# Optimization experiments

Measured on AMD Instinct MI355X. Metric: run time of the kernel, lower is better.

The kernel has to match this reference:

```python
import jax, jax.numpy as jnp
import numpy as np

# ---- module geometry ----
BULK = 64          # bulk (J2) integration points, 3 comps each
COH = 32           # cohesive integration points, 2 comps each
LS = BULK * 3 + COH * 2  # = 256, material layer width

# ---- J2 plasticity material constants (plane-stress, linear isotropic hardening) ----
E_MOD = 200.0
NU = 0.3
SY0 = 2.0
HARD = 10.0
G_MOD = E_MOD / (2.0 * (1.0 + NU))
_c = E_MOD / (1.0 - NU * NU)
C_EL = np.array([[_c, _c * NU, 0.0], [_c * NU, _c, 0.0], [0.0, 0.0, _c * (1.0 - NU) / 2.0]], dtype=np.float32)
C_INV = np.linalg.inv(C_EL).astype(np.float32)

# ---- Turon cohesive-zone constants (bilinear damage law) ----
K_PEN = 50.0       # penalty stiffness
DELTA0 = 0.1       # damage-onset effective jump
DELTAF = 1.0       # full-failure effective jump


def j2_update(eps, epsp, epbar):
    # eps, epsp: [B,P,3]; epbar: [B,P]. Radial-return with linear hardening.
    sig_tr = jnp.einsum('bpi,ji->bpj', eps - epsp, jnp.asarray(C_EL))
    s1, s2, s12 = sig_tr[..., 0], sig_tr[..., 1], sig_tr[..., 2]
    seq = jnp.sqrt(jnp.maximum(s1 * s1 - s1 * s2 + s2 * s2 + 3.0 * s12 * s12, 1e-12))
    f = seq - (SY0 + HARD * epbar)
    plastic = f > 0.0
    dep = jnp.where(plastic, f / (3.0 * G_MOD + HARD), 0.0)
    r = (SY0 + HARD * (epbar + dep)) / seq
    sig = jnp.where(plastic[..., None], r[..., None] * sig_tr, sig_tr)
    epsp_new = jnp.where(plastic[..., None], eps - jnp.einsum('bpj,ij->bpi', sig, jnp.asarray(C_INV)), epsp)
    return sig, epsp_new, epbar + dep


def coh_update(jump, hist):
    # jump: [B,P,2] (normal, shear); hist: [B,P] max effective jump (damage history).
    dn, ds = jump[..., 0], jump[..., 1]
    lam = jnp.sqrt(jnp.maximum(jnp.maximum(dn, 0.0) ** 2 + ds * ds, 1e-12))
    hist_new = jnp.maximum(hist, lam)
    dmg = jnp.clip(DELTAF * (hist_new - DELTA0) / (jnp.maximum(hist_new, 1e-12) * (DELTAF - DELTA0)), 0.0, 1.0)
    tn = K_PEN * dn * jnp.where(dn > 0.0, 1.0 - dmg, 1.0)  # compression is undamaged
    ts = (1.0 - dmg) * K_PEN * ds
    return jnp.stack([tn, ts], axis=-1), hist_new


def setup_inputs() -> dict:
    key = jax.random.key(0)
    k1, k2, k3 = jax.random.split(key, 3)
    x = jax.random.normal(k1, (256, 1024, 16), dtype=jnp.float32)
    W1 = jax.random.normal(k2, (LS, 16), dtype=jnp.float32) * 0.1
    W2 = jax.random.normal(k3, (16, LS), dtype=jnp.float32) * 0.1
    return {"x": x, "W1": W1, "W2": W2}


def reference(x, W1, W2):
    B, T, F = x.shape
    # fc1 applied to every (batch, time) slice (original loops; here one GEMM)
    h = jnp.einsum('btf,lf->btl', x, W1)  # [B,T,LS]
    h_t = jnp.transpose(h, (1, 0, 2))     # [T,B,LS] for the time scan

    epsp0 = jnp.zeros((B, BULK, 3), dtype=x.dtype)
    epbar0 = jnp.zeros((B, BULK), dtype=x.dtype)
    hist0 = jnp.zeros((B, COH), dtype=x.dtype)

    def step(carry, ht):
        epsp, epbar, hist = carry
        eps = ht[:, : BULK * 3].reshape(B, BULK, 3)
        jmp = ht[:, BULK * 3:].reshape(B, COH, 2)
        sig, epsp, epbar = j2_update(eps, epsp, epbar)   # update + commit per step
        trac, hist = coh_update(jmp, hist)
        y = jnp.concatenate([sig.reshape(B, -1), trac.reshape(B, -1)], axis=-1)
        return (epsp, epbar, hist), y

    _, ys = jax.lax.scan(step, (epsp0, epbar0, hist0), h_t)  # [T,B,LS]
    ys = jnp.transpose(ys, (1, 0, 2))  # [B,T,LS]
    # softLayer fc2: linear with softplus-constrained (non-negative) weights
    out = jnp.einsum('btl,ol->bto', ys, jax.nn.softplus(W2))
    return out
```

## Files before the change

kernel.cpp:

```cpp
#include <hip/hip_runtime.h>
#include <cmath>
#include <cstdint>

#define BATCH  256
#define TT     1024
#define FIN    16
#define LSZ    256
#define NBULK  64
#define NCOH   32
#define TC     32
#define NCHUNK (TT / TC)
#define HBS    260
#define HCS    68
#define YSS    336

typedef __attribute__((ext_vector_type(8))) short short8;
typedef __attribute__((ext_vector_type(4))) float floatx4;

__device__ __forceinline__ unsigned short f2bf_rne(float f) {
    union { float f; unsigned int i; } v; v.f = f;
    unsigned int b = v.i;
    return (unsigned short)((b + 0x7FFFu + ((b >> 16) & 1u)) >> 16);
}
__device__ __forceinline__ unsigned int bfbits(float f) {
    union { float f; unsigned int i; } v; v.f = f;
    return v.i + 0x8000u;
}

#define MC00   219.78021978021977f
#define MC01   65.93406593406593f
#define MC22   76.92307692307692f
#define MSY0   2.0f
#define AK     0.958466453674121406f
#define BK     0.041533546325878594f

__global__ __launch_bounds__(256, 1)
void fused_mat_kernel(const float* __restrict__ x,
                      const float* __restrict__ w1,
                      const float* __restrict__ w2,
                      float* __restrict__ out)
{
    __shared__ __attribute__((aligned(16))) float          s_hb[2][TC][HBS];
    __shared__ __attribute__((aligned(16))) float          s_hc[2][TC][HCS];
    __shared__ __attribute__((aligned(16))) unsigned short s_y [2][TC][YSS];

    const int tid  = threadIdx.x;
    const int b    = blockIdx.x;
    const int lane = tid & 63;
    const int wv   = tid >> 6;
    const int m    = lane & 15;
    const int q    = lane >> 4;

    const size_t xrow = (size_t)b * TT;

    short8 w1f[16];
    short8 vf[10];
    uint4  rxa[2], rxb[2];

    if (wv == 2) {
        #pragma unroll
        for (int n = 0; n < 16; ++n) {
            #pragma unroll
            for (int j = 0; j < 8; ++j) {
                unsigned short v = 0;
                if (q < 2) v = f2bf_rne(w1[(n * 16 + m) * FIN + q * 8 + j]);
                w1f[n][j] = (short)v;
            }
        }
        #pragma unroll
        for (int mt = 0; mt < 2; ++mt) {
            short8 a0;
            #pragma unroll
            for (int j = 0; j < 8; ++j) {
                unsigned short v = 0;
                if (q < 2) v = f2bf_rne(x[(xrow + mt * 16 + m) * FIN + q * 8 + j]);
                a0[j] = (short)v;
            }
            #pragma unroll
            for (int n = 0; n < 16; ++n) {
                floatx4 acc = {0.f, 0.f, 0.f, 0.f};
                acc = __builtin_amdgcn_mfma_f32_16x16x32_bf16(a0, w1f[n], acc, 0, 0, 0);
                const int col = n * 16 + m;
                if (n < 12) {
                    const int cc = col / 3, cm = col - cc * 3;
                    #pragma unroll
                    for (int r = 0; r < 4; ++r)
                        s_hb[0][mt * 16 + q * 4 + r][cc * 4 + cm] = acc[r];
                } else {
                    #pragma unroll
                    for (int r = 0; r < 4; ++r)
                        s_hc[0][mt * 16 + q * 4 + r][col - 192] = acc[r];
                }
            }
        }
        if (q < 2) {
            #pragma unroll
            for (int mt = 0; mt < 2; ++mt) {
                const float* xp = x + (xrow + TC + mt * 16 + m) * FIN + q * 8;
                rxa[mt] = *(const uint4*)xp;
                rxb[mt] = *(const uint4*)(xp + 4);
            }
        }
    } else if (wv == 3) {
        #pragma unroll
        for (int ks = 0; ks < 10; ++ks) {
            #pragma unroll
            for (int j = 0; j < 8; ++j) {
                const int p = ks * 32 + q * 8 + j;
                unsigned short v = 0;
                if (p < 256) {
                    const int comp = p & 3;
                    if (comp < 3) {
                        const int l = 3 * (p >> 2) + comp;
                        float xv = w2[m * LSZ + l];
                        float sp = fmaxf(xv, 0.0f) + log1pf(expf(-fabsf(xv)));
                        v = f2bf_rne(sp);
                    }
                } else {
                    const int l = p - 64;
                    float xv = w2[m * LSZ + l];
                    float sp = fmaxf(xv, 0.0f) + log1pf(expf(-fabsf(xv)));
                    v = f2bf_rne(sp);
                }
                vf[ks][j] = (short)v;
            }
        }
    }

    float sg0 = 0.f, sg1 = 0.f, sg2 = 0.f, syv = MSY0;
    float ep0 = 0.f, ep1 = 0.f, ep2 = 0.f;
    float hist = 0.f;

    __syncthreads();

    for (int i = 0; i <= NCHUNK; ++i) {
        if (wv == 0) {
            if (i < NCHUNK) {
                const float* hb = &s_hb[i & 1][0][0];
                floatx4 ev[TC];
                #pragma unroll
                for (int t = 0; t < TC; ++t)
                    ev[t] = *(const floatx4*)(hb + t * HBS + lane * 4);
                unsigned short* yb = &s_y[i & 1][0][0];
                #pragma unroll
                for (int t = 0; t < TC; ++t) {
                    const float e0 = ev[t].x, e1 = ev[t].y, e2 = ev[t].z;
                    const float d0 = e0 - ep0, d1 = e1 - ep1, d2 = e2 - ep2;
                    ep0 = e0; ep1 = e1; ep2 = e2;
                    const float dl0 = fmaf(MC01, d1, MC00 * d0);
                    const float dl1 = fmaf(MC00, d1, MC01 * d0);
                    const float dl2 = MC22 * d2;
                    const float pre = AK * syv;
                    const float t0 = sg0 + dl0, t1 = sg1 + dl1, t2 = sg2 + dl2;
                    const float a1 = t0 * (t0 - t1);
                    const float b1 = fmaf(t1, t1, 3.0f * (t2 * t2));
                    const float qq = fmaxf(a1 + b1, 1e-12f);
                    const float rs  = __builtin_amdgcn_rsqf(qq);
                    const float seq = qq * rs;
                    const float rr  = fminf(fmaf(pre, rs, BK), 1.0f);
                    sg0 = rr * t0; sg1 = rr * t1; sg2 = rr * t2;
                    syv = fmaf(BK, fmaxf(seq - syv, 0.0f), syv);
                    uint2 pk;
                    pk.x = (bfbits(sg0) >> 16) | (bfbits(sg1) & 0xFFFF0000u);
                    pk.y = (bfbits(sg2) >> 16);
                    *(uint2*)(yb + t * YSS + lane * 4) = pk;
                }
            }
        } else if (wv == 1) {
            if (i < NCHUNK && lane < NCOH) {
                const float* hc = &s_hc[i & 1][0][0];
                float2 jv[TC];
                #pragma unroll
                for (int t = 0; t < TC; ++t)
                    jv[t] = *(const float2*)(hc + t * HCS + 2 * lane);
                unsigned short* yb = &s_y[i & 1][0][0];
                #pragma unroll
                for (int t = 0; t < TC; ++t) {
                    const float dn = jv[t].x, ds = jv[t].y;
                    const float dnp = fmaxf(dn, 0.0f);
                    const float lam = sqrtf(fmaxf(fmaf(dnp, dnp, ds * ds), 1e-12f));
                    hist = fmaxf(hist, lam);
                    float dmg = (hist - 0.1f) * __builtin_amdgcn_rcpf(hist * 0.9f);
                    dmg = fminf(fmaxf(dmg, 0.0f), 1.0f);
                    const float om = 1.0f - dmg;
                    const float tn = 50.0f * dn * (dn > 0.0f ? om : 1.0f);
                    const float ts = om * 50.0f * ds;
                    unsigned int pk = (bfbits(tn) >> 16) | (bfbits(ts) & 0xFFFF0000u);
                    *(unsigned int*)(yb + t * YSS + 256 + 2 * lane) = pk;
                }
            }
        } else if (wv == 2) {
            if (i + 1 < NCHUNK) {
                short8 af[2];
                #pragma unroll
                for (int mt = 0; mt < 2; ++mt) {
                    const unsigned int w[8] = {rxa[mt].x, rxa[mt].y, rxa[mt].z, rxa[mt].w,
                                               rxb[mt].x, rxb[mt].y, rxb[mt].z, rxb[mt].w};
                    #pragma unroll
                    for (int j = 0; j < 8; ++j) {
                        unsigned short v = 0;
                        if (q < 2) {
                            union { unsigned int i; float f; } u; u.i = w[j];
                            v = f2bf_rne(u.f);
                        }
                        af[mt][j] = (short)v;
                    }
                }
                if (i + 2 < NCHUNK && q < 2) {
                    #pragma unroll
                    for (int mt = 0; mt < 2; ++mt) {
                        const float* xp = x + (xrow + (i + 2) * TC + mt * 16 + m) * FIN + q * 8;
                        rxa[mt] = *(const uint4*)xp;
                        rxb[mt] = *(const uint4*)(xp + 4);
                    }
                }
                float* hbw = &s_hb[(i + 1) & 1][0][0];
                float* hcw = &s_hc[(i + 1) & 1][0][0];
                #pragma unroll
                for (int mt = 0; mt < 2; ++mt) {
                    #pragma unroll
                    for (int n = 0; n < 16; ++n) {
                        floatx4 acc = {0.f, 0.f, 0.f, 0.f};
                        acc = __builtin_amdgcn_mfma_f32_16x16x32_bf16(af[mt], w1f[n], acc, 0, 0, 0);
                        const int col = n * 16 + m;
                        if (n < 12) {
                            const int cc = col / 3, cm = col - cc * 3;
                            #pragma unroll
                            for (int r = 0; r < 4; ++r)
                                hbw[(mt * 16 + q * 4 + r) * HBS + cc * 4 + cm] = acc[r];
                        } else {
                            #pragma unroll
                            for (int r = 0; r < 4; ++r)
                                hcw[(mt * 16 + q * 4 + r) * HCS + col - 192] = acc[r];
                        }
                    }
                }
            }
        } else {
            if (i >= 1) {
                const int t0 = (i - 1) * TC;
                const unsigned short* yb = &s_y[(i - 1) & 1][0][0];
                #pragma unroll
                for (int mt = 0; mt < 2; ++mt) {
                    floatx4 a0 = {0.f, 0.f, 0.f, 0.f};
                    floatx4 a1 = {0.f, 0.f, 0.f, 0.f};
                    #pragma unroll
                    for (int ks = 0; ks < 5; ++ks) {
                        const short8* yp = (const short8*)(yb + (mt * 16 + m) * YSS + ks * 32 + q * 8);
                        a0 = __builtin_amdgcn_mfma_f32_16x16x32_bf16(*yp, vf[ks], a0, 0, 0, 0);
                    }
                    #pragma unroll
                    for (int ks = 5; ks < 10; ++ks) {
                        const short8* yp = (const short8*)(yb + (mt * 16 + m) * YSS + ks * 32 + q * 8);
                        a1 = __builtin_amdgcn_mfma_f32_16x16x32_bf16(*yp, vf[ks], a1, 0, 0, 0);
                    }
                    #pragma unroll
                    for (int r = 0; r < 4; ++r)
                        out[(xrow + t0 + mt * 16 + q * 4 + r) * FIN + m] = a0[r] + a1[r];
                }
            }
        }
        __syncthreads();
    }
}

extern "C" void kernel_launch(void* const* d_in, const int* in_sizes, int n_in,
                              void* d_out, int out_size, void* d_ws, size_t ws_size,
                              hipStream_t stream) {
    const float* x  = (const float*)d_in[0];
    const float* w1 = (const float*)d_in[1];
    const float* w2 = (const float*)d_in[2];
    float* out = (float*)d_out;
    fused_mat_kernel<<<BATCH, 256, 0, stream>>>(x, w1, w2, out);
}
```

Measured before the change: 174.6 us.

## Pack two batch rows per block and shrink time chunk to 16

Each 512-thread block now handles two batch rows with independent four-wave pipelines, and the time chunk drops from 32 to 16 steps. Output stores are deferred by one chunk so they overlap the next MFMA step, and the cohesive sqrt uses the hardware builtin. The intent is to keep the serial recurrence waves busier and shorten the per-chunk latency, which lowers pipeline fill cost. In exchange there are twice as many block-wide barriers, and 128 blocks may leave some compute units idle.

```diff
diff --git a/kernel.cpp b/kernel.cpp
--- a/kernel.cpp
+++ b/kernel.cpp
@@ -8,7 +8,7 @@
 #define LSZ    256
 #define NBULK  64
 #define NCOH   32
-#define TC     32
+#define TC     16
 #define NCHUNK (TT / TC)
 #define HBS    260
 #define HCS    68
@@ -34,30 +34,32 @@
 #define AK     0.958466453674121406f
 #define BK     0.041533546325878594f
 
-__global__ __launch_bounds__(256, 1)
+__global__ __launch_bounds__(512, 1)
 void fused_mat_kernel(const float* __restrict__ x,
                       const float* __restrict__ w1,
                       const float* __restrict__ w2,
                       float* __restrict__ out)
 {
-    __shared__ __attribute__((aligned(16))) float          s_hb[2][TC][HBS];
-    __shared__ __attribute__((aligned(16))) float          s_hc[2][TC][HCS];
-    __shared__ __attribute__((aligned(16))) unsigned short s_y [2][TC][YSS];
+    __shared__ __attribute__((aligned(16))) float          s_hb[2][2][TC][HBS];
+    __shared__ __attribute__((aligned(16))) float          s_hc[2][2][TC][HCS];
+    __shared__ __attribute__((aligned(16))) unsigned short s_y [2][2][TC][YSS];
 
     const int tid  = threadIdx.x;
-    const int b    = blockIdx.x;
     const int lane = tid & 63;
-    const int wv   = tid >> 6;
+    const int wv8  = tid >> 6;
+    const int p    = wv8 >> 2;
+    const int role = wv8 & 3;
     const int m    = lane & 15;
     const int q    = lane >> 4;
 
+    const int b = blockIdx.x * 2 + p;
     const size_t xrow = (size_t)b * TT;
 
     short8 w1f[16];
     short8 vf[10];
-    uint4  rxa[2], rxb[2];
-
-    if (wv == 2) {
+    uint4  rxa, rxb;
+
+    if (role == 2) {
         #pragma unroll
         for (int n = 0; n < 16; ++n) {
             #pragma unroll
@@ -67,57 +69,51 @@
                 w1f[n][j] = (short)v;
             }
         }
-        #pragma unroll
-        for (int mt = 0; mt < 2; ++mt) {
-            short8 a0;
-            #pragma unroll
-            for (int j = 0; j < 8; ++j) {
-                unsigned short v = 0;
-                if (q < 2) v = f2bf_rne(x[(xrow + mt * 16 + m) * FIN + q * 8 + j]);
-                a0[j] = (short)v;
-            }
-            #pragma unroll
-            for (int n = 0; n < 16; ++n) {
-                floatx4 acc = {0.f, 0.f, 0.f, 0.f};
-                acc = __builtin_amdgcn_mfma_f32_16x16x32_bf16(a0, w1f[n], acc, 0, 0, 0);
-                const int col = n * 16 + m;
-                if (n < 12) {
-                    const int cc = col / 3, cm = col - cc * 3;
-                    #pragma unroll
-                    for (int r = 0; r < 4; ++r)
-                        s_hb[0][mt * 16 + q * 4 + r][cc * 4 + cm] = acc[r];
-                } else {
-                    #pragma unroll
-                    for (int r = 0; r < 4; ++r)
-                        s_hc[0][mt * 16 + q * 4 + r][col - 192] = acc[r];
-                }
+        short8 a0;
+        #pragma unroll
+        for (int j = 0; j < 8; ++j) {
+            unsigned short v = 0;
+            if (q < 2) v = f2bf_rne(x[(xrow + m) * FIN + q * 8 + j]);
+            a0[j] = (short)v;
+        }
+        #pragma unroll
+        for (int n = 0; n < 16; ++n) {
+            floatx4 acc = {0.f, 0.f, 0.f, 0.f};
+            acc = __builtin_amdgcn_mfma_f32_16x16x32_bf16(a0, w1f[n], acc, 0, 0, 0);
+            const int col = n * 16 + m;
+            if (n < 12) {
+                const int cc = col / 3, cm = col - cc * 3;
+                #pragma unroll
+                for (int r = 0; r < 4; ++r)
+                    s_hb[p][0][q * 4 + r][cc * 4 + cm] = acc[r];
+            } else {
+                #pragma unroll
+                for (int r = 0; r < 4; ++r)
+                    s_hc[p][0][q * 4 + r][col - 192] = acc[r];
             }
         }
         if (q < 2) {
-            #pragma unroll
-            for (int mt = 0; mt < 2; ++mt) {
-                const float* xp = x + (xrow + TC + mt * 16 + m) * FIN + q * 8;
-                rxa[mt] = *(const uint4*)xp;
-                rxb[mt] = *(const uint4*)(xp + 4);
-            }
-        }
-    } else if (wv == 3) {
+            const float* xp = x + (xrow + TC + m) * FIN + q * 8;
+            rxa = *(const uint4*)xp;
+            rxb = *(const uint4*)(xp + 4);
+        }
+    } else if (role == 3) {
         #pragma unroll
         for (int ks = 0; ks < 10; ++ks) {
             #pragma unroll
             for (int j = 0; j < 8; ++j) {
-                const int p = ks * 32 + q * 8 + j;
+                const int pp = ks * 32 + q * 8 + j;
                 unsigned short v = 0;
-                if (p < 256) {
-                    const int comp = p & 3;
+                if (pp < 256) {
+                    const int comp = pp & 3;
                     if (comp < 3) {
-                        const int l = 3 * (p >> 2) + comp;
+                        const int l = 3 * (pp >> 2) + comp;
                         float xv = w2[m * LSZ + l];
                         float sp = fmaxf(xv, 0.0f) + log1pf(expf(-fabsf(xv)));
                         v = f2bf_rne(sp);
                     }
                 } else {
-                    const int l = p - 64;
+                    const int l = pp - 64;
                     float xv = w2[m * LSZ + l];
                     float sp = fmaxf(xv, 0.0f) + log1pf(expf(-fabsf(xv)));
                     v = f2bf_rne(sp);
@@ -130,18 +126,20 @@
     float sg0 = 0.f, sg1 = 0.f, sg2 = 0.f, syv = MSY0;
     float ep0 = 0.f, ep1 = 0.f, ep2 = 0.f;
     float hist = 0.f;
+    floatx4 sacc = {0.f, 0.f, 0.f, 0.f};
 
     __syncthreads();
 
     for (int i = 0; i <= NCHUNK; ++i) {
-        if (wv == 0) {
+        if (role == 0) {
             if (i < NCHUNK) {
-                const float* hb = &s_hb[i & 1][0][0];
+                const float* hb = &s_hb[p][i & 1][0][0];
+                unsigned short* yb = &s_y[p][i & 1][0][0];
+                const int off = lane * 4;
                 floatx4 ev[TC];
                 #pragma unroll
                 for (int t = 0; t < TC; ++t)
-                    ev[t] = *(const floatx4*)(hb + t * HBS + lane * 4);
-                unsigned short* yb = &s_y[i & 1][0][0];
+                    ev[t] = *(const floatx4*)(hb + t * HBS + off);
                 #pragma unroll
                 for (int t = 0; t < TC; ++t) {
                     const float e0 = ev[t].x, e1 = ev[t].y, e2 = ev[t].z;
@@ -163,22 +161,23 @@
                     uint2 pk;
                     pk.x = (bfbits(sg0) >> 16) | (bfbits(sg1) & 0xFFFF0000u);
                     pk.y = (bfbits(sg2) >> 16);
-                    *(uint2*)(yb + t * YSS + lane * 4) = pk;
-                }
-            }
-        } else if (wv == 1) {
+                    *(uint2*)(yb + t * YSS + off) = pk;
+                }
+            }
+        } else if (role == 1) {
             if (i < NCHUNK && lane < NCOH) {
-                const float* hc = &s_hc[i & 1][0][0];
+                const float* hc = &s_hc[p][i & 1][0][0];
+                unsigned short* yb = &s_y[p][i & 1][0][0];
+                const int off = 2 * lane;
                 float2 jv[TC];
                 #pragma unroll
                 for (int t = 0; t < TC; ++t)
-                    jv[t] = *(const float2*)(hc + t * HCS + 2 * lane);
-                unsigned short* yb = &s_y[i & 1][0][0];
+                    jv[t] = *(const float2*)(hc + t * HCS + off);
                 #pragma unroll
                 for (int t = 0; t < TC; ++t) {
                     const float dn = jv[t].x, ds = jv[t].y;
                     const float dnp = fmaxf(dn, 0.0f);
-                    const float lam = sqrtf(fmaxf(fmaf(dnp, dnp, ds * ds), 1e-12f));
+                    const float lam = __builtin_amdgcn_sqrtf(fmaxf(fmaf(dnp, dnp, ds * ds), 1e-12f));
                     hist = fmaxf(hist, lam);
                     float dmg = (hist - 0.1f) * __builtin_amdgcn_rcpf(hist * 0.9f);
                     dmg = fminf(fmaxf(dmg, 0.0f), 1.0f);
@@ -186,16 +185,15 @@
                     const float tn = 50.0f * dn * (dn > 0.0f ? om : 1.0f);
                     const float ts = om * 50.0f * ds;
                     unsigned int pk = (bfbits(tn) >> 16) | (bfbits(ts) & 0xFFFF0000u);
-                    *(unsigned int*)(yb + t * YSS + 256 + 2 * lane) = pk;
-                }
-            }
-        } else if (wv == 2) {
+                    *(unsigned int*)(yb + t * YSS + 256 + off) = pk;
+                }
+            }
+        } else if (role == 2) {
             if (i + 1 < NCHUNK) {
-                short8 af[2];
-                #pragma unroll
-                for (int mt = 0; mt < 2; ++mt) {
-                    const unsigned int w[8] = {rxa[mt].x, rxa[mt].y, rxa[mt].z, rxa[mt].w,
-                                               rxb[mt].x, rxb[mt].y, rxb[mt].z, rxb[mt].w};
+                short8 af;
+                {
+                    const unsigned int w[8] = {rxa.x, rxa.y, rxa.z, rxa.w,
+                                               rxb.x, rxb.y, rxb.z, rxb.w};
                     #pragma unroll
                     for (int j = 0; j < 8; ++j) {
                         unsigned short v = 0;
@@ -203,64 +201,66 @@
                             union { unsigned int i; float f; } u; u.i = w[j];
                             v = f2bf_rne(u.f);
                         }
-                        af[mt][j] = (short)v;
+                        af[j] = (short)v;
                     }
                 }
                 if (i + 2 < NCHUNK && q < 2) {
-                    #pragma unroll
-                    for (int mt = 0; mt < 2; ++mt) {
-                        const float* xp = x + (xrow + (i + 2) * TC + mt * 16 + m) * FIN + q * 8;
-                        rxa[mt] = *(const uint4*)xp;
-                        rxb[mt] = *(const uint4*)(xp + 4);
+                    const float* xp = x + (xrow + (i + 2) * TC + m) * FIN + q * 8;
+                    rxa = *(const uint4*)xp;
+                    rxb = *(const uint4*)(xp + 4);
+                }
+                float* hbw = &s_hb[p][(i + 1) & 1][0][0];
+                float* hcw = &s_hc[p][(i + 1) & 1][0][0];
+                #pragma unroll
+                for (int n = 0; n < 16; ++n) {
+                    floatx4 acc = {0.f, 0.f, 0.f, 0.f};
+                    acc = __builtin_amdgcn_mfma_f32_16x16x32_bf16(af, w1f[n], acc, 0, 0, 0);
+                    const int col = n * 16 + m;
+                    if (n < 12) {
+                        const int cc = col / 3, cm = col - cc * 3;
+                        #pragma unroll
+                        for (int r = 0; r < 4; ++r)
+                            hbw[(q * 4 + r) * HBS + cc * 4 + cm] = acc[r];
+                    } else {
+                        #pragma unroll
+                        for (int r = 0; r < 4; ++r)
+                            hcw[(q * 4 + r) * HCS + col - 192] = acc[r];
                     }
                 }
-                float* hbw = &s_hb[(i + 1) & 1][0][0];
-                float* hcw = &s_hc[(i + 1) & 1][0][0];
-                #pragma unroll
-                for (int mt = 0; mt < 2; ++mt) {
-                    #pragma unroll
-                    for (int n = 0; n < 16; ++n) {
-                        floatx4 acc = {0.f, 0.f, 0.f, 0.f};
-                        acc = __builtin_amdgcn_mfma_f32_16x16x32_bf16(af[mt], w1f[n], acc, 0, 0, 0);
-                        const int col = n * 16 + m;
-                        if (n < 12) {
-                            const int cc = col / 3, cm = col - cc * 3;
-                            #pragma unroll
-                            for (int r = 0; r < 4; ++r)
-                                hbw[(mt * 16 + q * 4 + r) * HBS + cc * 4 + cm] = acc[r];
-                        } else {
-                            #pragma unroll
-                            for (int r = 0; r < 4; ++r)
-                                hcw[(mt * 16 + q * 4 + r) * HCS + col - 192] = acc[r];
-                        }
-                    }
-                }
             }
         } else {
-            if (i >= 1) {
-                const int t0 = (i - 1) * TC;
-                const unsigned short* yb = &s_y[(i - 1) & 1][0][0];
-                #pragma unroll
-                for (int mt = 0; mt < 2; ++mt) {
-                    floatx4 a0 = {0.f, 0.f, 0.f, 0.f};
-                    floatx4 a1 = {0.f, 0.f, 0.f, 0.f};
-                    #pragma unroll
-                    for (int ks = 0; ks < 5; ++ks) {
-                        const short8* yp = (const short8*)(yb + (mt * 16 + m) * YSS + ks * 32 + q * 8);
-                        a0 = __builtin_amdgcn_mfma_f32_16x16x32_bf16(*yp, vf[ks], a0, 0, 0, 0);
-                    }
-                    #pragma unroll
-                    for (int ks = 5; ks < 10; ++ks) {
-                        const short8* yp = (const short8*)(yb + (mt * 16 + m) * YSS + ks * 32 + q * 8);
-                        a1 = __builtin_amdgcn_mfma_f32_16x16x32_bf16(*yp, vf[ks], a1, 0, 0, 0);
-                    }
-                    #pragma unroll
-                    for (int r = 0; r < 4; ++r)
-                        out[(xrow + t0 + mt * 16 + q * 4 + r) * FIN + m] = a0[r] + a1[r];
-                }
+            if (i >= 2) {
+                const int t0 = (i - 2) * TC;
+                #pragma unroll
+                for (int r = 0; r < 4; ++r)
+                    out[(xrow + t0 + q * 4 + r) * FIN + m] = sacc[r];
+            }
+            if (i >= 1 && i <= NCHUNK) {
+                const unsigned short* yb = &s_y[p][(i - 1) & 1][0][0];
+                floatx4 a0 = {0.f, 0.f, 0.f, 0.f};
+                floatx4 a1 = {0.f, 0.f, 0.f, 0.f};
+                #pragma unroll
+                for (int ks = 0; ks < 5; ++ks) {
+                    const short8* yp = (const short8*)(yb + m * YSS + ks * 32 + q * 8);
+                    a0 = __builtin_amdgcn_mfma_f32_16x16x32_bf16(*yp, vf[ks], a0, 0, 0, 0);
+                }
+                #pragma unroll
+                for (int ks = 5; ks < 10; ++ks) {
+                    const short8* yp = (const short8*)(yb + m * YSS + ks * 32 + q * 8);
+                    a1 = __builtin_amdgcn_mfma_f32_16x16x32_bf16(*yp, vf[ks], a1, 0, 0, 0);
+                }
+                #pragma unroll
+                for (int r = 0; r < 4; ++r) sacc[r] = a0[r] + a1[r];
             }
         }
         __syncthreads();
+    }
+
+    if (role == 3) {
+        const int t0 = (NCHUNK - 1) * TC;
+        #pragma unroll
+        for (int r = 0; r < 4; ++r)
+            out[(xrow + t0 + q * 4 + r) * FIN + m] = sacc[r];
     }
 }
 
@@ -271,5 +271,5 @@
     const float* w1 = (const float*)d_in[1];
     const float* w2 = (const float*)d_in[2];
     float* out = (float*)d_out;
-    fused_mat_kernel<<<BATCH, 256, 0, stream>>>(x, w1, w2, out);
-}
+    fused_mat_kernel<<<BATCH / 2, 512, 0, stream>>>(x, w1, w2, out);
+}
```

New measurement: 222.6 us. +27.5%, slower.

## Fold elastic stiffness and time differencing into fc1 weights for the J2 path

Applied to the files above, without the earlier changes.

Precomputes W1 premultiplied by the elastic stiffness matrix and feeds the MFMA the time difference of x, so the producer wave writes strain-increment stress deltas straight to shared memory. The serial J2 wave then skips the per-step subtraction and 3x3 stiffness multiply, which shortens the critical recurrence. The history arrays in registers are replaced by per-step LDS loads, the cohesive sqrt uses the hardware builtin, and the barrier becomes an inline waitcnt plus s_barrier. The cost is double x loads in the producer wave and rounding x-differences and scaled weights to bf16, which changes numerical error, possibly accumulating in the stress recurrence.

```diff
diff --git a/kernel.cpp b/kernel.cpp
--- a/kernel.cpp
+++ b/kernel.cpp
@@ -26,6 +26,11 @@
     union { float f; unsigned int i; } v; v.f = f;
     return v.i + 0x8000u;
 }
+__device__ __forceinline__ float u2f(unsigned int u) {
+    union { unsigned int i; float f; } v; v.i = u; return v.f;
+}
+
+#define BARRIER() asm volatile("s_waitcnt lgkmcnt(0)\n\ts_barrier" ::: "memory")
 
 #define MC00   219.78021978021977f
 #define MC01   65.93406593406593f
@@ -53,33 +58,58 @@
 
     const size_t xrow = (size_t)b * TT;
 
-    short8 w1f[16];
+    short8 w1fd[12];
+    short8 w1f4[4];
     short8 vf[10];
-    uint4  rxa[2], rxb[2];
+    uint4  rxc[2][2], rxp[2][2];
 
     if (wv == 2) {
         #pragma unroll
-        for (int n = 0; n < 16; ++n) {
+        for (int n = 0; n < 12; ++n) {
+            #pragma unroll
+            for (int j = 0; j < 8; ++j) {
+                float v = 0.f;
+                if (q < 2) {
+                    const int l = n * 16 + m, c = l / 3, cm = l - 3 * c, f = q * 8 + j;
+                    const float wa = w1[(3 * c + 0) * FIN + f];
+                    const float wb = w1[(3 * c + 1) * FIN + f];
+                    const float wc = w1[(3 * c + 2) * FIN + f];
+                    v = (cm == 0) ? fmaf(MC01, wb, MC00 * wa)
+                      : (cm == 1) ? fmaf(MC00, wb, MC01 * wa)
+                                  : MC22 * wc;
+                }
+                w1fd[n][j] = (short)f2bf_rne(v);
+            }
+        }
+        #pragma unroll
+        for (int n = 12; n < 16; ++n) {
             #pragma unroll
             for (int j = 0; j < 8; ++j) {
                 unsigned short v = 0;
                 if (q < 2) v = f2bf_rne(w1[(n * 16 + m) * FIN + q * 8 + j]);
-                w1f[n][j] = (short)v;
+                w1f4[n - 12][j] = (short)v;
             }
         }
         #pragma unroll
         for (int mt = 0; mt < 2; ++mt) {
-            short8 a0;
+            short8 ax, adx;
             #pragma unroll
             for (int j = 0; j < 8; ++j) {
-                unsigned short v = 0;
-                if (q < 2) v = f2bf_rne(x[(xrow + mt * 16 + m) * FIN + q * 8 + j]);
-                a0[j] = (short)v;
+                float xc = 0.f, xp = 0.f;
+                if (q < 2) {
+                    const int rowB = mt * 16 + m;
+                    xc = x[(xrow + rowB) * FIN + q * 8 + j];
+                    if (rowB > 0) xp = x[(xrow + rowB - 1) * FIN + q * 8 + j];
+                }
+                ax[j]  = (short)f2bf_rne(xc);
+                adx[j] = (short)f2bf_rne(xc - xp);
             }
             #pragma unroll
             for (int n = 0; n < 16; ++n) {
                 floatx4 acc = {0.f, 0.f, 0.f, 0.f};
-                acc = __builtin_amdgcn_mfma_f32_16x16x32_bf16(a0, w1f[n], acc, 0, 0, 0);
+                acc = (n < 12)
+                    ? __builtin_amdgcn_mfma_f32_16x16x32_bf16(adx, w1fd[n], acc, 0, 0, 0)
+                    : __builtin_amdgcn_mfma_f32_16x16x32_bf16(ax, w1f4[n - 12], acc, 0, 0, 0);
                 const int col = n * 16 + m;
                 if (n < 12) {
                     const int cc = col / 3, cm = col - cc * 3;
@@ -96,9 +126,11 @@
         if (q < 2) {
             #pragma unroll
             for (int mt = 0; mt < 2; ++mt) {
-                const float* xp = x + (xrow + TC + mt * 16 + m) * FIN + q * 8;
-                rxa[mt] = *(const uint4*)xp;
-                rxb[mt] = *(const uint4*)(xp + 4);
+                const int rowB = TC + mt * 16 + m;
+                const float* xc = x + (xrow + rowB) * FIN + q * 8;
+                const float* xp = x + (xrow + rowB - 1) * FIN + q * 8;
+                rxc[mt][0] = *(const uint4*)xc;  rxc[mt][1] = *(const uint4*)(xc + 4);
+                rxp[mt][0] = *(const uint4*)xp;  rxp[mt][1] = *(const uint4*)(xp + 4);
             }
         }
     } else if (wv == 3) {
@@ -128,7 +160,6 @@
     }
 
     float sg0 = 0.f, sg1 = 0.f, sg2 = 0.f, syv = MSY0;
-    float ep0 = 0.f, ep1 = 0.f, ep2 = 0.f;
     float hist = 0.f;
 
     __syncthreads();
@@ -137,21 +168,13 @@
         if (wv == 0) {
             if (i < NCHUNK) {
                 const float* hb = &s_hb[i & 1][0][0];
-                floatx4 ev[TC];
-                #pragma unroll
-                for (int t = 0; t < TC; ++t)
-                    ev[t] = *(const floatx4*)(hb + t * HBS + lane * 4);
                 unsigned short* yb = &s_y[i & 1][0][0];
+                const int off = lane * 4;
                 #pragma unroll
                 for (int t = 0; t < TC; ++t) {
-                    const float e0 = ev[t].x, e1 = ev[t].y, e2 = ev[t].z;
-                    const float d0 = e0 - ep0, d1 = e1 - ep1, d2 = e2 - ep2;
-                    ep0 = e0; ep1 = e1; ep2 = e2;
-                    const float dl0 = fmaf(MC01, d1, MC00 * d0);
-                    const float dl1 = fmaf(MC00, d1, MC01 * d0);
-                    const float dl2 = MC22 * d2;
+                    const floatx4 dv = *(const floatx4*)(hb + t * HBS + off);
                     const float pre = AK * syv;
-                    const float t0 = sg0 + dl0, t1 = sg1 + dl1, t2 = sg2 + dl2;
+                    const float t0 = sg0 + dv.x, t1 = sg1 + dv.y, t2 = sg2 + dv.z;
                     const float a1 = t0 * (t0 - t1);
                     const float b1 = fmaf(t1, t1, 3.0f * (t2 * t2));
                     const float qq = fmaxf(a1 + b1, 1e-12f);
@@ -163,22 +186,20 @@
                     uint2 pk;
                     pk.x = (bfbits(sg0) >> 16) | (bfbits(sg1) & 0xFFFF0000u);
                     pk.y = (bfbits(sg2) >> 16);
-                    *(uint2*)(yb + t * YSS + lane * 4) = pk;
+                    *(uint2*)(yb + t * YSS + off) = pk;
                 }
             }
         } else if (wv == 1) {
             if (i < NCHUNK && lane < NCOH) {
                 const float* hc = &s_hc[i & 1][0][0];
-                float2 jv[TC];
-                #pragma unroll
-                for (int t = 0; t < TC; ++t)
-                    jv[t] = *(const float2*)(hc + t * HCS + 2 * lane);
                 unsigned short* yb = &s_y[i & 1][0][0];
+                const int off = 2 * lane;
                 #pragma unroll
                 for (int t = 0; t < TC; ++t) {
-                    const float dn = jv[t].x, ds = jv[t].y;
+                    const float2 jv = *(const float2*)(hc + t * HCS + off);
+                    const float dn = jv.x, ds = jv.y;
                     const float dnp = fmaxf(dn, 0.0f);
-                    const float lam = sqrtf(fmaxf(fmaf(dnp, dnp, ds * ds), 1e-12f));
+                    const float lam = __builtin_amdgcn_sqrtf(fmaxf(fmaf(dnp, dnp, ds * ds), 1e-12f));
                     hist = fmaxf(hist, lam);
                     float dmg = (hist - 0.1f) * __builtin_amdgcn_rcpf(hist * 0.9f);
                     dmg = fminf(fmaxf(dmg, 0.0f), 1.0f);
@@ -186,32 +207,38 @@
                     const float tn = 50.0f * dn * (dn > 0.0f ? om : 1.0f);
                     const float ts = om * 50.0f * ds;
                     unsigned int pk = (bfbits(tn) >> 16) | (bfbits(ts) & 0xFFFF0000u);
-                    *(unsigned int*)(yb + t * YSS + 256 + 2 * lane) = pk;
+                    *(unsigned int*)(yb + t * YSS + 256 + off) = pk;
                 }
             }
         } else if (wv == 2) {
             if (i + 1 < NCHUNK) {
-                short8 af[2];
+                short8 ax[2], adx[2];
                 #pragma unroll
                 for (int mt = 0; mt < 2; ++mt) {
-                    const unsigned int w[8] = {rxa[mt].x, rxa[mt].y, rxa[mt].z, rxa[mt].w,
-                                               rxb[mt].x, rxb[mt].y, rxb[mt].z, rxb[mt].w};
+                    const unsigned int wc[8] = {rxc[mt][0].x, rxc[mt][0].y, rxc[mt][0].z, rxc[mt][0].w,
+                                                rxc[mt][1].x, rxc[mt][1].y, rxc[mt][1].z, rxc[mt][1].w};
+                    const unsigned int wp[8] = {rxp[mt][0].x, rxp[mt][0].y, rxp[mt][0].z, rxp[mt][0].w,
+                                                rxp[mt][1].x, rxp[mt][1].y, rxp[mt][1].z, rxp[mt][1].w};
                     #pragma unroll
                     for (int j = 0; j < 8; ++j) {
-                        unsigned short v = 0;
+                        unsigned short va = 0, vd = 0;
                         if (q < 2) {
-                            union { unsigned int i; float f; } u; u.i = w[j];
-                            v = f2bf_rne(u.f);
+                            const float xc = u2f(wc[j]), xp = u2f(wp[j]);
+                            va = f2bf_rne(xc);
+                            vd = f2bf_rne(xc - xp);
                         }
-                        af[mt][j] = (short)v;
+                        ax[mt][j]  = (short)va;
+                        adx[mt][j] = (short)vd;
                     }
                 }
                 if (i + 2 < NCHUNK && q < 2) {
                     #pragma unroll
                     for (int mt = 0; mt < 2; ++mt) {
-                        const float* xp = x + (xrow + (i + 2) * TC + mt * 16 + m) * FIN + q * 8;
-                        rxa[mt] = *(const uint4*)xp;
-                        rxb[mt] = *(const uint4*)(xp + 4);
+                        const int rowB = (i + 2) * TC + mt * 16 + m;
+                        const float* xc = x + (xrow + rowB) * FIN + q * 8;
+                        const float* xp = x + (xrow + rowB - 1) * FIN + q * 8;
+                        rxc[mt][0] = *(const uint4*)xc;  rxc[mt][1] = *(const uint4*)(xc + 4);
+                        rxp[mt][0] = *(const uint4*)xp;  rxp[mt][1] = *(const uint4*)(xp + 4);
                     }
                 }
                 float* hbw = &s_hb[(i + 1) & 1][0][0];
@@ -221,7 +248,9 @@
                     #pragma unroll
                     for (int n = 0; n < 16; ++n) {
                         floatx4 acc = {0.f, 0.f, 0.f, 0.f};
-                        acc = __builtin_amdgcn_mfma_f32_16x16x32_bf16(af[mt], w1f[n], acc, 0, 0, 0);
+                        acc = (n < 12)
+                            ? __builtin_amdgcn_mfma_f32_16x16x32_bf16(adx[mt], w1fd[n], acc, 0, 0, 0)
+                            : __builtin_amdgcn_mfma_f32_16x16x32_bf16(ax[mt], w1f4[n - 12], acc, 0, 0, 0);
                         const int col = n * 16 + m;
                         if (n < 12) {
                             const int cc = col / 3, cm = col - cc * 3;
@@ -260,7 +289,7 @@
                 }
             }
         }
-        __syncthreads();
+        BARRIER();
     }
 }
 
```

Result: faster. 160.6 us (-8.0%).
